# Kernel optimization log

Hardware: AMD Instinct MI355X
Metric: run time of the kernel (lower is better)

Reference implementation:

```python
import jax, jax.numpy as jnp
import numpy as np

# Topology constants (size='medium')
N_SW = 131      # 49 + 32 + 24 + 16 + 10
N_L = 64        # n_wavelengths
N_M = 32        # n_modes
PS = 4          # patch_size
V1_START, V1_COUNT = 0, 49
OUT_START, OUT_COUNT = 121, 10
DECAY = 0.15


def _encode(images):
    # images: [B, 28, 28] -> patches [B, 49, 16] -> pad to n_modes -> [B, 49, 64, 32]
    B = images.shape[0]
    p = images[:, :28, :28].reshape(B, 7, PS, 7, PS)
    p = p.transpose(0, 1, 3, 2, 4).reshape(B, 49, PS * PS)
    p = jnp.pad(p, ((0, 0), (0, 0), (0, N_M - PS * PS)))
    w_idx = jnp.arange(N_L, dtype=jnp.float32)
    w_weights = 1.0 - jnp.abs(w_idx - 32.0) / 64.0
    return p[:, :, None, :] * w_weights[None, None, :, None]


def _phase_step(field_r, field_i, out_r, out_i, conn_r, conn_i, phase, gain_sp):
    # Complex gather over switch graph: contract source switch dim s against conn[s, t]
    g_r = jnp.einsum('bsLm,st->btLm', out_r, conn_r) - jnp.einsum('bsLm,st->btLm', out_i, conn_i)
    g_i = jnp.einsum('bsLm,st->btLm', out_r, conn_i) + jnp.einsum('bsLm,st->btLm', out_i, conn_r)
    cp = jnp.cos(phase)[None, :, None, None]
    sp = jnp.sin(phase)[None, :, None, None]
    gr = g_r * cp - g_i * sp
    gi = g_r * sp + g_i * cp
    field_r = field_r * (1.0 - DECAY) + gr * 0.25
    field_i = field_i * (1.0 - DECAY) + gi * 0.25
    mag = jnp.sqrt(field_r ** 2 + field_i ** 2 + 1e-8)
    new_mag = jnp.tanh(mag * gain_sp[None, :, None, None])
    scale = new_mag / (mag + 1e-8)
    return field_r, field_i, field_r * scale, field_i * scale


def setup_inputs() -> dict:
    key = jax.random.key(0)
    k_img, k_mag, k_ph, k_w = jax.random.split(key, 4)
    images = jax.random.normal(k_img, (128, 28, 28), dtype=jnp.float32)
    conn_mag = jnp.abs(jax.random.normal(k_mag, (N_SW, N_SW), dtype=jnp.float32)) * 0.03
    conn_phase = jax.random.normal(k_ph, (N_SW, N_SW), dtype=jnp.float32) * 0.1
    conn_real = conn_mag * jnp.cos(conn_phase)
    conn_imag = conn_mag * jnp.sin(conn_phase)
    switch_phase = jnp.zeros((N_SW,), dtype=jnp.float32)
    switch_gain = jnp.ones((N_SW,), dtype=jnp.float32)
    readout_w = jax.random.normal(k_w, (10, OUT_COUNT), dtype=jnp.float32) * 0.1
    readout_b = jnp.zeros((10,), dtype=jnp.float32)
    return {
        'images': images,
        'conn_real': conn_real,
        'conn_imag': conn_imag,
        'switch_phase': switch_phase,
        'switch_gain': switch_gain,
        'readout_w': readout_w,
        'readout_b': readout_b,
        'n_steps': 10,
        'injection_steps': 4,
    }


def reference(images, conn_real, conn_imag, switch_phase, switch_gain,
              readout_w, readout_b, n_steps, injection_steps):
    enc = _encode(images)
    enc_max = jnp.max(jnp.abs(enc))
    enc = enc * jnp.where(enc_max > 1e-8, 1.0 / enc_max, 1.0)
    B = images.shape[0]
    field_r = jnp.zeros((B, N_SW, N_L, N_M), dtype=images.dtype)
    field_i = jnp.zeros_like(field_r)
    out_r = jnp.zeros_like(field_r)
    out_i = jnp.zeros_like(field_r)
    gain_sp = jax.nn.softplus(switch_gain)
    inj = enc * 0.3  # [B, 49, 64, 32], goes into V1 slots
    for t in range(n_steps):
        if t < injection_steps:
            field_r = field_r.at[:, V1_START:V1_START + V1_COUNT].add(inj)
        field_r, field_i, out_r, out_i = _phase_step(
            field_r, field_i, out_r, out_i, conn_real, conn_imag, switch_phase, gain_sp)
    orr = out_r[:, OUT_START:OUT_START + OUT_COUNT]
    oii = out_i[:, OUT_START:OUT_START + OUT_COUNT]
    energy = (orr ** 2 + oii ** 2).sum(axis=(2, 3))
    features = jnp.log1p(energy + 1e-8)
    return features @ readout_w.T + readout_b
```

## Files before the change

### kernel.cpp

```cpp
#include <hip/hip_runtime.h>
#include <cmath>


#define NSTEPS  10
#define INJ_ST  4
#define MT      144
#define NTASK   4224

typedef __bf16 bf16x8 __attribute__((ext_vector_type(8)));
typedef __bf16 bf16x4 __attribute__((ext_vector_type(4)));
typedef short  short8 __attribute__((ext_vector_type(8)));
typedef float  f32x4  __attribute__((ext_vector_type(4)));

#define WS_MAX    0
#define WS_ENERGY 64
#define WS_GSP    2048
#define WS_CONN   4096

__global__ void k_pre(const float* __restrict__ img,
                      const float* __restrict__ cr, const float* __restrict__ ci,
                      const float* __restrict__ phase, const float* __restrict__ gain,
                      float* ws) {
    if (blockIdx.x < 98) {
        __shared__ float sm[256];
        float v = 0.f;
        for (int i = blockIdx.x * 256 + threadIdx.x; i < 128 * 28 * 28; i += 98 * 256)
            v = fmaxf(v, fabsf(img[i]));
        sm[threadIdx.x] = v;
        __syncthreads();
        for (int s = 128; s > 0; s >>= 1) {
            if (threadIdx.x < s) sm[threadIdx.x] = fmaxf(sm[threadIdx.x], sm[threadIdx.x + s]);
            __syncthreads();
        }
        if (threadIdx.x == 0)
            atomicMax((unsigned int*)(ws + WS_MAX), __float_as_uint(sm[0]));
        return;
    }
    int i = (blockIdx.x - 98) * 256 + threadIdx.x;
    __bf16* Cb = (__bf16*)(ws + WS_CONN);
    const int NCE = MT * 160;
    if (i < NCE) {
        int m = i / 160, k = i % 160;
        float vr = 0.f, vi = 0.f;
        if (m < 131 && k < 131) {
            float a = cr[k * 131 + m], b = ci[k * 131 + m];
            float ph = phase[m];
            float cp = cosf(ph), sp = sinf(ph);
            vr = a * cp - b * sp;
            vi = a * sp + b * cp;
        }
        int ca = ((k >> 3) * MT + m) * 8 + (k & 7);
        Cb[ca]       = (__bf16)vr;
        Cb[NCE + ca] = (__bf16)vi;
    } else if (i < NCE + MT) {
        int j = i - NCE;
        float g = 0.f;
        if (j < 131) {
            float x = gain[j];
            g = (x > 20.f) ? x : log1pf(expf(x));
        }
        ws[WS_GSP + j] = g * -0.72134754543f;
    }
}

static __device__ __forceinline__ f32x4 MF(bf16x8 a, bf16x8 b, f32x4 c) {
    return __builtin_amdgcn_mfma_f32_16x16x32_bf16(a, b, c, 0, 0, 0);
}
static __device__ __forceinline__ bf16x8 bneg(bf16x8 a) {
    short8 t = __builtin_bit_cast(short8, a) ^ (short8)(short)0x8000;
    return __builtin_bit_cast(bf16x8, t);
}

#define CPAIR(AR, AI, BR, BI, BNI, P)                                  \
    accr[P] = MF(AR, BR,  accr[P]);                                    \
    accr[P] = MF(AI, BNI, accr[P]);                                    \
    acci[P] = MF(AR, BI,  acci[P]);                                    \
    acci[P] = MF(AI, BR,  acci[P]);

__global__ __launch_bounds__(512, 2)
void k_main(const float* __restrict__ img, const float* __restrict__ ws,
            float* __restrict__ energy) {
    __shared__ __bf16 CrL[18 * MT * 8];
    __shared__ __bf16 CiL[18 * MT * 8];
    __shared__ __bf16 OBP[2][8][18 * 16 * 8];
    __shared__ float  gspL[144];

    const int tid  = threadIdx.x;
    const int lane = tid & 63;
    const int ln15 = lane & 15;
    const int quad = lane >> 4;
    const int w    = __builtin_amdgcn_readfirstlane(tid >> 6);

    __bf16* __restrict__ OWr = &OBP[0][w][0];
    __bf16* __restrict__ OWi = &OBP[1][w][0];

    const float mx = ws[WS_MAX];
    const float sc = (mx > 1e-8f) ? (1.02f / mx) : 1.02f;

    {
        const int4* srcR = (const int4*)(ws + WS_CONN);
        const int4* srcI = (const int4*)(ws + WS_CONN + (MT * 160 / 2));
        int4* dstR = (int4*)CrL;
        int4* dstI = (int4*)CiL;
        for (int i = tid; i < 2592; i += 512) { dstR[i] = srcR[i]; dstI[i] = srcI[i]; }
        if (tid < 144) gspL[tid] = ws[WS_GSP + tid];
    }
    __syncthreads();

#pragma unroll 1
    for (int r = 0; r < 3; ++r) {
        const int T = r * 2048 + blockIdx.x * 8 + w;
        if (T >= NTASK) break;
        const int u  = T >> 7;
        const int im = T & 127;
        const float wl  = 1.0f - fabsf((float)u - 32.0f) * (1.0f / 64.0f);
        const float wgt = (u == 0 || u == 32) ? 1.0f : 2.0f;
        const int imgb = im * 784 + (ln15 >> 2) * 28 + (ln15 & 3);

        f32x4 accr[9], acci[9];
#pragma unroll
        for (int p = 0; p < 9; ++p) { accr[p] = (f32x4)0.f; acci[p] = (f32x4)0.f; }

        auto inj_add = [&]() {
#pragma unroll
            for (int mt = 0; mt < 4; ++mt) {
#pragma unroll
                for (int rr = 0; rr < 4; ++rr) {
                    int j = mt * 16 + quad * 4 + rr;
                    if (j < 49) {
                        int pi = j / 7, pj = j % 7;
                        float px = img[imgb + pi * 112 + pj * 4];
                        float t  = px * sc;
                        accr[mt][rr] = fmaf(t, wl, accr[mt][rr]);
                    }
                }
            }
        };

        auto epilogue = [&]() {
#pragma unroll
            for (int mt = 0; mt < 9; ++mt) {
                f32x4 g2v = *(const f32x4*)(gspL + mt * 16 + quad * 4);
                bf16x4 pr, pi;
#pragma unroll
                for (int rr = 0; rr < 4; ++rr) {
                    float ar = accr[mt][rr], ai = acci[mt][rr];
                    float mag2 = fmaf(ar, ar, fmaf(ai, ai, 1.6e-7f));
                    float rsq  = __builtin_amdgcn_rsqf(mag2);
                    float e    = __builtin_amdgcn_exp2f(g2v[rr] * (mag2 * rsq));
                    float uu   = __builtin_amdgcn_rcpf(1.0f + e);
                    float th   = fmaf(-2.0f, e * uu, 1.0f);
                    float scv  = th * rsq;
                    pr[rr] = (__bf16)(ar * scv); pi[rr] = (__bf16)(ai * scv);
                }
                const int off = ((mt * 2 + (quad >> 1)) * 16 + ln15) * 8
                              + (quad & 1) * 4;
                *(bf16x4*)(OWr + off) = pr;
                *(bf16x4*)(OWi + off) = pi;
            }
        };

        inj_add();
        epilogue();

#pragma unroll 1
        for (int t = 1; t < NSTEPS - 1; ++t) {
#pragma unroll
            for (int p = 0; p < 9; ++p) { accr[p] *= 0.85f; acci[p] *= 0.85f; }
            if (t < INJ_ST) inj_add();

            const int ktEnd = (t == 1) ? 2 : 5;
#pragma unroll 1
            for (int kt = 0; kt < ktEnd; ++kt) {
                const int kch = kt * 4 + quad;
                const int rk  = (kch > 17) ? 17 : kch;
                const int bb  = (rk * 16 + ln15) * 8;
                bf16x8 br = *(const bf16x8*)(OWr + bb);
                bf16x8 bi = *(const bf16x8*)(OWi + bb);
                const int ab = (rk * MT + ln15) * 8;
                bf16x8 ar[9], ai[9];
#pragma unroll
                for (int mt = 0; mt < 9; ++mt) {
                    ar[mt] = *(const bf16x8*)(CrL + ab + mt * 128);
                    ai[mt] = *(const bf16x8*)(CiL + ab + mt * 128);
                }
                bf16x8 bn = bneg(bi);
#pragma unroll
                for (int mt = 0; mt < 9; ++mt) {
                    CPAIR(ar[mt], ai[mt], br, bi, bn, mt)
                }
            }
            epilogue();
        }

        accr[7] *= 0.85f; acci[7] *= 0.85f;
        accr[8] *= 0.85f; acci[8] *= 0.85f;
#pragma unroll 1
        for (int kt = 0; kt < 5; ++kt) {
            const int kch = kt * 4 + quad;
            const int rk  = (kch > 17) ? 17 : kch;
            const int bb  = (rk * 16 + ln15) * 8;
            bf16x8 br = *(const bf16x8*)(OWr + bb);
            bf16x8 bi = *(const bf16x8*)(OWi + bb);
            const int ab = (rk * MT + ln15) * 8;
            bf16x8 ar7 = *(const bf16x8*)(CrL + ab + 7 * 128);
            bf16x8 ai7 = *(const bf16x8*)(CiL + ab + 7 * 128);
            bf16x8 ar8 = *(const bf16x8*)(CrL + ab + 8 * 128);
            bf16x8 ai8 = *(const bf16x8*)(CiL + ab + 8 * 128);
            bf16x8 bn = bneg(bi);
            CPAIR(ar7, ai7, br, bi, bn, 7)
            CPAIR(ar8, ai8, br, bi, bn, 8)
        }

#pragma unroll
        for (int mt = 7; mt < 9; ++mt) {
#pragma unroll
            for (int rr = 0; rr < 4; ++rr) {
                int j = mt * 16 + quad * 4 + rr;
                if (j >= 121 && j <= 130) {
                    float ar = accr[mt][rr], ai = acci[mt][rr];
                    float mag2 = fmaf(ar, ar, fmaf(ai, ai, 1.6e-7f));
                    float rsq  = __builtin_amdgcn_rsqf(mag2);
                    float e    = __builtin_amdgcn_exp2f(gspL[j] * (mag2 * rsq));
                    float uu   = __builtin_amdgcn_rcpf(1.0f + e);
                    float th   = fmaf(-2.0f, e * uu, 1.0f);
                    float scv  = th * rsq;
                    float orv = ar * scv, oiv = ai * scv;
                    float e2 = orv * orv + oiv * oiv;
                    e2 += __shfl_xor(e2, 1);
                    e2 += __shfl_xor(e2, 2);
                    e2 += __shfl_xor(e2, 4);
                    e2 += __shfl_xor(e2, 8);
                    if (ln15 == 0)
                        atomicAdd(energy + im * 10 + (j - 121), e2 * wgt);
                }
            }
        }
    }
}

__global__ void k_readout(const float* __restrict__ ws,
                          const float* __restrict__ W,
                          const float* __restrict__ bias,
                          float* __restrict__ out) {
    int i = blockIdx.x * 256 + threadIdx.x;
    if (i < 1280) {
        int b = i / 10, o = i % 10;
        float s = bias[o];
#pragma unroll
        for (int f = 0; f < 10; ++f) {
            float feat = log1pf(ws[WS_ENERGY + b * 10 + f] + 1e-8f);
            s = fmaf(feat, W[o * 10 + f], s);
        }
        out[i] = s;
    }
}

extern "C" void kernel_launch(void* const* d_in, const int* in_sizes, int n_in,
                              void* d_out, int out_size, void* d_ws, size_t ws_size,
                              hipStream_t stream) {
    const float* images = (const float*)d_in[0];
    const float* conn_r = (const float*)d_in[1];
    const float* conn_i = (const float*)d_in[2];
    const float* phase  = (const float*)d_in[3];
    const float* gain   = (const float*)d_in[4];
    const float* W      = (const float*)d_in[5];
    const float* bias   = (const float*)d_in[6];
    float* ws  = (float*)d_ws;
    float* out = (float*)d_out;

    hipMemsetAsync(ws, 0, (WS_ENERGY + 1280) * sizeof(float), stream);
    hipLaunchKernelGGL(k_pre, dim3(189), dim3(256), 0, stream,
                       images, conn_r, conn_i, phase, gain, ws);
    hipLaunchKernelGGL(k_main, dim3(256), dim3(512), 0, stream,
                       images, ws, ws + WS_ENERGY);
    hipLaunchKernelGGL(k_readout, dim3(5), dim3(256), 0, stream, ws, W, bias, out);
}
```

Measured before the change: 217.7 us.

## Hold first three K-chunks of connection matrix in registers with fewer waves

Each wave now preloads the connection-matrix fragments for the first three K-chunks (54 bf16x8 values) into registers once, so they are not re-read from LDS on every step. Only the remaining two K-chunks still come from LDS each step. To make room for those registers, the block shrinks to 256 threads with one block per SM, and each wave works through up to five tasks instead of three. The risk is lower occupancy and less latency hiding, and possible register spilling from the large register-resident arrays.

```diff
diff --git a/kernel.cpp b/kernel.cpp
--- a/kernel.cpp
+++ b/kernel.cpp
@@ -77,12 +77,12 @@
     acci[P] = MF(AR, BI,  acci[P]);                                    \
     acci[P] = MF(AI, BR,  acci[P]);
 
-__global__ __launch_bounds__(512, 2)
+__global__ __launch_bounds__(256, 1)
 void k_main(const float* __restrict__ img, const float* __restrict__ ws,
             float* __restrict__ energy) {
     __shared__ __bf16 CrL[18 * MT * 8];
     __shared__ __bf16 CiL[18 * MT * 8];
-    __shared__ __bf16 OBP[2][8][18 * 16 * 8];
+    __shared__ __bf16 OBP[2][4][18 * 16 * 8];
     __shared__ float  gspL[144];
 
     const int tid  = threadIdx.x;
@@ -102,14 +102,25 @@
         const int4* srcI = (const int4*)(ws + WS_CONN + (MT * 160 / 2));
         int4* dstR = (int4*)CrL;
         int4* dstI = (int4*)CiL;
-        for (int i = tid; i < 2592; i += 512) { dstR[i] = srcR[i]; dstI[i] = srcI[i]; }
+        for (int i = tid; i < 2592; i += 256) { dstR[i] = srcR[i]; dstI[i] = srcI[i]; }
         if (tid < 144) gspL[tid] = ws[WS_GSP + tid];
     }
     __syncthreads();
 
+    bf16x8 cR[3][9], cI[3][9];
+#pragma unroll
+    for (int kt = 0; kt < 3; ++kt) {
+        const int ab = ((kt * 4 + quad) * MT + ln15) * 8;
+#pragma unroll
+        for (int mt = 0; mt < 9; ++mt) {
+            cR[kt][mt] = *(const bf16x8*)(CrL + ab + mt * 128);
+            cI[kt][mt] = *(const bf16x8*)(CiL + ab + mt * 128);
+        }
+    }
+
 #pragma unroll 1
-    for (int r = 0; r < 3; ++r) {
-        const int T = r * 2048 + blockIdx.x * 8 + w;
+    for (int r = 0; r < 5; ++r) {
+        const int T = r * 1024 + blockIdx.x * 4 + w;
         if (T >= NTASK) break;
         const int u  = T >> 7;
         const int im = T & 127;
@@ -169,25 +180,50 @@
             for (int p = 0; p < 9; ++p) { accr[p] *= 0.85f; acci[p] *= 0.85f; }
             if (t < INJ_ST) inj_add();
 
-            const int ktEnd = (t == 1) ? 2 : 5;
+            if (t == 1) {
+#pragma unroll
+                for (int kt = 0; kt < 2; ++kt) {
+                    const int bb = ((kt * 4 + quad) * 16 + ln15) * 8;
+                    bf16x8 br = *(const bf16x8*)(OWr + bb);
+                    bf16x8 bi = *(const bf16x8*)(OWi + bb);
+                    bf16x8 bn = bneg(bi);
+#pragma unroll
+                    for (int mt = 0; mt < 9; ++mt) {
+                        CPAIR(cR[kt][mt], cI[kt][mt], br, bi, bn, mt)
+                    }
+                }
+            } else {
+#pragma unroll
+                for (int kt = 0; kt < 3; ++kt) {
+                    const int bb = ((kt * 4 + quad) * 16 + ln15) * 8;
+                    bf16x8 br = *(const bf16x8*)(OWr + bb);
+                    bf16x8 bi = *(const bf16x8*)(OWi + bb);
+                    bf16x8 bn = bneg(bi);
+#pragma unroll
+                    for (int mt = 0; mt < 9; ++mt) {
+                        CPAIR(cR[kt][mt], cI[kt][mt], br, bi, bn, mt)
+                    }
+                }
+                __builtin_amdgcn_sched_barrier(0);
 #pragma unroll 1
-            for (int kt = 0; kt < ktEnd; ++kt) {
-                const int kch = kt * 4 + quad;
-                const int rk  = (kch > 17) ? 17 : kch;
-                const int bb  = (rk * 16 + ln15) * 8;
-                bf16x8 br = *(const bf16x8*)(OWr + bb);
-                bf16x8 bi = *(const bf16x8*)(OWi + bb);
-                const int ab = (rk * MT + ln15) * 8;
-                bf16x8 ar[9], ai[9];
-#pragma unroll
-                for (int mt = 0; mt < 9; ++mt) {
-                    ar[mt] = *(const bf16x8*)(CrL + ab + mt * 128);
-                    ai[mt] = *(const bf16x8*)(CiL + ab + mt * 128);
-                }
-                bf16x8 bn = bneg(bi);
-#pragma unroll
-                for (int mt = 0; mt < 9; ++mt) {
-                    CPAIR(ar[mt], ai[mt], br, bi, bn, mt)
+                for (int kt = 3; kt < 5; ++kt) {
+                    const int kch = kt * 4 + quad;
+                    const int rk  = (kch > 17) ? 17 : kch;
+                    const int bb  = (rk * 16 + ln15) * 8;
+                    bf16x8 br = *(const bf16x8*)(OWr + bb);
+                    bf16x8 bi = *(const bf16x8*)(OWi + bb);
+                    const int ab = (rk * MT + ln15) * 8;
+                    bf16x8 ar[9], ai[9];
+#pragma unroll
+                    for (int mt = 0; mt < 9; ++mt) {
+                        ar[mt] = *(const bf16x8*)(CrL + ab + mt * 128);
+                        ai[mt] = *(const bf16x8*)(CiL + ab + mt * 128);
+                    }
+                    bf16x8 bn = bneg(bi);
+#pragma unroll
+                    for (int mt = 0; mt < 9; ++mt) {
+                        CPAIR(ar[mt], ai[mt], br, bi, bn, mt)
+                    }
                 }
             }
             epilogue();
@@ -195,8 +231,18 @@
 
         accr[7] *= 0.85f; acci[7] *= 0.85f;
         accr[8] *= 0.85f; acci[8] *= 0.85f;
+#pragma unroll
+        for (int kt = 0; kt < 3; ++kt) {
+            const int bb = ((kt * 4 + quad) * 16 + ln15) * 8;
+            bf16x8 br = *(const bf16x8*)(OWr + bb);
+            bf16x8 bi = *(const bf16x8*)(OWi + bb);
+            bf16x8 bn = bneg(bi);
+            CPAIR(cR[kt][7], cI[kt][7], br, bi, bn, 7)
+            CPAIR(cR[kt][8], cI[kt][8], br, bi, bn, 8)
+        }
+        __builtin_amdgcn_sched_barrier(0);
 #pragma unroll 1
-        for (int kt = 0; kt < 5; ++kt) {
+        for (int kt = 3; kt < 5; ++kt) {
             const int kch = kt * 4 + quad;
             const int rk  = (kch > 17) ? 17 : kch;
             const int bb  = (rk * 16 + ln15) * 8;
@@ -272,7 +318,7 @@
     hipMemsetAsync(ws, 0, (WS_ENERGY + 1280) * sizeof(float), stream);
     hipLaunchKernelGGL(k_pre, dim3(189), dim3(256), 0, stream,
                        images, conn_r, conn_i, phase, gain, ws);
-    hipLaunchKernelGGL(k_main, dim3(256), dim3(512), 0, stream,
+    hipLaunchKernelGGL(k_main, dim3(256), dim3(256), 0, stream,
                        images, ws, ws + WS_ENERGY);
     hipLaunchKernelGGL(k_readout, dim3(5), dim3(256), 0, stream, ws, W, bias, out);
 }
```

Result: slower. 245.5 us (+12.8%).

## Use nine waves per block and trim padded K chunk to one quad

Applied to the files above, without the earlier changes.

Raises the block size from 8 to 9 wavefronts so the 4224 tasks finish in two rounds instead of three. LDS buffers shrink from 18 to 17 K-chunks so nine waves still fit. The last K chunk (chunk 16) is now handled by a dedicated routine where only quad 0 loads real data and the others feed zeros. This removes the clamped duplicate chunks of the old fifth K iteration. It also skips writing the out-of-range padded rows in the epilogue. The trade-off is higher per-block LDS and thread count, which could affect occupancy at two blocks per CU, plus extra branching in the tail MFMA routine.

```diff
diff --git a/kernel.cpp b/kernel.cpp
--- a/kernel.cpp
+++ b/kernel.cpp
@@ -77,12 +77,12 @@
     acci[P] = MF(AR, BI,  acci[P]);                                    \
     acci[P] = MF(AI, BR,  acci[P]);
 
-__global__ __launch_bounds__(512, 2)
+__global__ __launch_bounds__(576, 2)
 void k_main(const float* __restrict__ img, const float* __restrict__ ws,
             float* __restrict__ energy) {
-    __shared__ __bf16 CrL[18 * MT * 8];
-    __shared__ __bf16 CiL[18 * MT * 8];
-    __shared__ __bf16 OBP[2][8][18 * 16 * 8];
+    __shared__ __bf16 CrL[17 * MT * 8];
+    __shared__ __bf16 CiL[17 * MT * 8];
+    __shared__ __bf16 OBP[2][9][17 * 16 * 8];
     __shared__ float  gspL[144];
 
     const int tid  = threadIdx.x;
@@ -102,14 +102,16 @@
         const int4* srcI = (const int4*)(ws + WS_CONN + (MT * 160 / 2));
         int4* dstR = (int4*)CrL;
         int4* dstI = (int4*)CiL;
-        for (int i = tid; i < 2592; i += 512) { dstR[i] = srcR[i]; dstI[i] = srcI[i]; }
+        for (int i = tid; i < 2448; i += 576) { dstR[i] = srcR[i]; dstI[i] = srcI[i]; }
         if (tid < 144) gspL[tid] = ws[WS_GSP + tid];
     }
     __syncthreads();
 
+    const bf16x8 zf = __builtin_bit_cast(bf16x8, (short8)(short)0);
+
 #pragma unroll 1
-    for (int r = 0; r < 3; ++r) {
-        const int T = r * 2048 + blockIdx.x * 8 + w;
+    for (int r = 0; r < 2; ++r) {
+        const int T = r * 2304 + blockIdx.x * 9 + w;
         if (T >= NTASK) break;
         const int u  = T >> 7;
         const int im = T & 127;
@@ -153,11 +155,46 @@
                     float scv  = th * rsq;
                     pr[rr] = (__bf16)(ar * scv); pi[rr] = (__bf16)(ai * scv);
                 }
-                const int off = ((mt * 2 + (quad >> 1)) * 16 + ln15) * 8
-                              + (quad & 1) * 4;
-                *(bf16x4*)(OWr + off) = pr;
-                *(bf16x4*)(OWi + off) = pi;
-            }
+                if (mt < 8 || (quad >> 1) == 0) {
+                    const int off = ((mt * 2 + (quad >> 1)) * 16 + ln15) * 8
+                                  + (quad & 1) * 4;
+                    *(bf16x4*)(OWr + off) = pr;
+                    *(bf16x4*)(OWi + off) = pi;
+                }
+            }
+        };
+
+        auto kt4_mfma = [&](bool full) {
+            bf16x8 br = zf, bi = zf, a7r = zf, a7i = zf, a8r = zf, a8i = zf;
+            bf16x8 ar[7], ai[7];
+#pragma unroll
+            for (int mt = 0; mt < 7; ++mt) { ar[mt] = zf; ai[mt] = zf; }
+            if (quad == 0) {
+                const int bb = (16 * 16 + ln15) * 8;
+                br = *(const bf16x8*)(OWr + bb);
+                bi = *(const bf16x8*)(OWi + bb);
+                const int ab = (16 * MT + ln15) * 8;
+                if (full) {
+#pragma unroll
+                    for (int mt = 0; mt < 7; ++mt) {
+                        ar[mt] = *(const bf16x8*)(CrL + ab + mt * 128);
+                        ai[mt] = *(const bf16x8*)(CiL + ab + mt * 128);
+                    }
+                }
+                a7r = *(const bf16x8*)(CrL + ab + 7 * 128);
+                a7i = *(const bf16x8*)(CiL + ab + 7 * 128);
+                a8r = *(const bf16x8*)(CrL + ab + 8 * 128);
+                a8i = *(const bf16x8*)(CiL + ab + 8 * 128);
+            }
+            bf16x8 bn = bneg(bi);
+            if (full) {
+#pragma unroll
+                for (int mt = 0; mt < 7; ++mt) {
+                    CPAIR(ar[mt], ai[mt], br, bi, bn, mt)
+                }
+            }
+            CPAIR(a7r, a7i, br, bi, bn, 7)
+            CPAIR(a8r, a8i, br, bi, bn, 8)
         };
 
         inj_add();
@@ -169,12 +206,11 @@
             for (int p = 0; p < 9; ++p) { accr[p] *= 0.85f; acci[p] *= 0.85f; }
             if (t < INJ_ST) inj_add();
 
-            const int ktEnd = (t == 1) ? 2 : 5;
+            const int ktEnd = (t == 1) ? 2 : 4;
 #pragma unroll 1
             for (int kt = 0; kt < ktEnd; ++kt) {
-                const int kch = kt * 4 + quad;
-                const int rk  = (kch > 17) ? 17 : kch;
-                const int bb  = (rk * 16 + ln15) * 8;
+                const int rk = kt * 4 + quad;
+                const int bb = (rk * 16 + ln15) * 8;
                 bf16x8 br = *(const bf16x8*)(OWr + bb);
                 bf16x8 bi = *(const bf16x8*)(OWi + bb);
                 const int ab = (rk * MT + ln15) * 8;
@@ -190,16 +226,16 @@
                     CPAIR(ar[mt], ai[mt], br, bi, bn, mt)
                 }
             }
+            if (t > 1) kt4_mfma(true);
             epilogue();
         }
 
         accr[7] *= 0.85f; acci[7] *= 0.85f;
         accr[8] *= 0.85f; acci[8] *= 0.85f;
 #pragma unroll 1
-        for (int kt = 0; kt < 5; ++kt) {
-            const int kch = kt * 4 + quad;
-            const int rk  = (kch > 17) ? 17 : kch;
-            const int bb  = (rk * 16 + ln15) * 8;
+        for (int kt = 0; kt < 4; ++kt) {
+            const int rk = kt * 4 + quad;
+            const int bb = (rk * 16 + ln15) * 8;
             bf16x8 br = *(const bf16x8*)(OWr + bb);
             bf16x8 bi = *(const bf16x8*)(OWi + bb);
             const int ab = (rk * MT + ln15) * 8;
@@ -211,6 +247,7 @@
             CPAIR(ar7, ai7, br, bi, bn, 7)
             CPAIR(ar8, ai8, br, bi, bn, 8)
         }
+        kt4_mfma(false);
 
 #pragma unroll
         for (int mt = 7; mt < 9; ++mt) {
@@ -272,7 +309,7 @@
     hipMemsetAsync(ws, 0, (WS_ENERGY + 1280) * sizeof(float), stream);
     hipLaunchKernelGGL(k_pre, dim3(189), dim3(256), 0, stream,
                        images, conn_r, conn_i, phase, gain, ws);
-    hipLaunchKernelGGL(k_main, dim3(256), dim3(512), 0, stream,
+    hipLaunchKernelGGL(k_main, dim3(256), dim3(576), 0, stream,
                        images, ws, ws + WS_ENERGY);
     hipLaunchKernelGGL(k_readout, dim3(5), dim3(256), 0, stream, ws, W, bias, out);
 }
```

Result: slower. 260.0 us (+19.4%).
